# Optimization experiments

Measured on AMD Instinct MI355X. Metric: run time of the kernel, lower is better.

## Reference

```python
import jax, jax.numpy as jnp
import numpy as np
import math

E = 1024
H = 16
D = E // H  # 64
B, T, S = 4, 1024, 1024


def setup_inputs() -> dict:
    key = jax.random.key(0)
    ks = jax.random.split(key, 10)
    sd = 1.0 / math.sqrt(D)
    se = 1.0 / math.sqrt(E)
    return {
        "query": jax.random.normal(ks[0], (B, T, E), jnp.float32),
        "paragraph_encoding": jax.random.normal(ks[1], (S, E), jnp.float32),
        "Wq": jax.random.normal(ks[2], (D, D), jnp.float32) * sd,
        "bq": jax.random.normal(ks[3], (D,), jnp.float32) * sd,
        "Wk": jax.random.normal(ks[4], (D, D), jnp.float32) * sd,
        "bk": jax.random.normal(ks[5], (D,), jnp.float32) * sd,
        "Wv": jax.random.normal(ks[6], (D, D), jnp.float32) * sd,
        "bv": jax.random.normal(ks[7], (D,), jnp.float32) * sd,
        "Wout": jax.random.normal(ks[8], (E, E), jnp.float32) * se,
        "bout": jax.random.normal(ks[9], (E,), jnp.float32) * se,
    }


def reference(query, paragraph_encoding, Wq, bq, Wk, bk, Wv, bv, Wout, bout):
    b, t, _ = query.shape
    s = paragraph_encoding.shape[0]
    # [B, H, T, D]
    q = query.reshape(b, t, H, D).transpose(0, 2, 1, 3)
    # [H, S, D] -- key/value shared across batch
    p = paragraph_encoding.reshape(s, H, D).transpose(1, 0, 2)
    # per-head linear projections (torch Linear: x @ W.T + b)
    q = q @ Wq.T + bq
    k = p @ Wk.T + bk
    v = p @ Wv.T + bv
    # scores scaled by sqrt(embed_size), NOT head_dim (faithful to source)
    scores = jnp.einsum("bhtd,hsd->bhts", q, k) / math.sqrt(E)
    attn = jax.nn.softmax(scores, axis=-1)
    # (mask is None in this configuration; masking would occur AFTER softmax)
    context = jnp.einsum("bhts,hsd->bhtd", attn, v)
    context = context.transpose(0, 2, 1, 3).reshape(b, t, E)
    return context @ Wout.T + bout
```

## Files before the change

kernel.cpp:

```cpp
#include <hip/hip_runtime.h>


typedef __attribute__((ext_vector_type(8))) short short8v;
typedef __attribute__((ext_vector_type(4))) short short4v;
typedef __attribute__((ext_vector_type(4))) float float4v;

#define MFMA_BF16(A, B, C) __builtin_amdgcn_mfma_f32_16x16x32_bf16(A, B, C, 0, 0, 0)

#if __has_builtin(__builtin_amdgcn_exp2f)
#define EXP2F(x) __builtin_amdgcn_exp2f(x)
#else
#define EXP2F(x) exp2f(x)
#endif

#define QSCALE 0.045084220027780106f

__device__ __forceinline__ short f2bf(float f) {
  union { float f; unsigned u; } v; v.f = f;
  unsigned r = v.u + 0x7FFFu + ((v.u >> 16) & 1u);
  return (short)(r >> 16);
}

__device__ __forceinline__ unsigned cvt_pk_bf16(float lo, float hi) {
  unsigned r;
  asm("v_cvt_pk_bf16_f32 %0, %1, %2" : "=v"(r) : "v"(lo), "v"(hi));
  return r;
}

__global__ __launch_bounds__(256) void proj_qkv(
    const float* __restrict__ query, const float* __restrict__ para,
    const float* __restrict__ Wq, const float* __restrict__ bq,
    const float* __restrict__ Wk, const float* __restrict__ bk,
    const float* __restrict__ Wv, const float* __restrict__ bv,
    const float* __restrict__ Wout,
    short* __restrict__ qs, short* __restrict__ kb, short* __restrict__ vt,
    short* __restrict__ wb) {
  const int task = blockIdx.x * 4 + (threadIdx.x >> 6);
  const int lane = threadIdx.x & 63;
  const int g = lane >> 4, c = lane & 15;

  if (task >= 6144) {
    const int j = task - 6144;
    const float* src = Wout + j * 2048;
    short* dst = wb + j * 2048;
#pragma unroll
    for (int it = 0; it < 4; ++it) {
      const int off = it * 512 + lane * 8;
      float4v x0 = *(const float4v*)(src + off);
      float4v x1 = *(const float4v*)(src + off + 4);
      short8v v = (short8v){ f2bf(x0.x), f2bf(x0.y), f2bf(x0.z), f2bf(x0.w),
                             f2bf(x1.x), f2bf(x1.y), f2bf(x1.z), f2bf(x1.w) };
      *(short8v*)(dst + off) = v;
    }
    return;
  }

  const float* W;
  const float* bias;
  const float* xrow;
  int type, h, tile, bh = 0;
  if (task < 4096) {
    type = 0; bh = task >> 6; tile = task & 63; h = bh & 15;
    xrow = query + ((bh >> 4) * 1024 + tile * 16 + c) * 1024 + h * 64;
    W = Wq; bias = bq;
  } else if (task < 5120) {
    int idx = task - 4096;
    type = 1; h = idx >> 6; tile = idx & 63;
    xrow = para + (tile * 16 + c) * 1024 + h * 64;
    W = Wk; bias = bk;
  } else {
    int idx = task - 5120;
    type = 2; h = idx >> 6; tile = idx & 63;
    xrow = para + (tile * 16 + c) * 1024 + h * 64;
    W = Wv; bias = bv;
  }

  short8v af[2];
#pragma unroll
  for (int kh = 0; kh < 2; ++kh) {
    const float* xp = xrow + kh * 32 + g * 8;
    float4v x0 = *(const float4v*)xp;
    float4v x1 = *(const float4v*)(xp + 4);
    af[kh] = (short8v){ f2bf(x0.x), f2bf(x0.y), f2bf(x0.z), f2bf(x0.w),
                        f2bf(x1.x), f2bf(x1.y), f2bf(x1.z), f2bf(x1.w) };
  }

#pragma unroll
  for (int dn = 0; dn < 4; ++dn) {
    float4v acc = (float4v){0.f, 0.f, 0.f, 0.f};
#pragma unroll
    for (int kh = 0; kh < 2; ++kh) {
      const float* wp = W + (dn * 16 + c) * 64 + kh * 32 + g * 8;
      float4v w0 = *(const float4v*)wp;
      float4v w1 = *(const float4v*)(wp + 4);
      short8v bfr = (short8v){ f2bf(w0.x), f2bf(w0.y), f2bf(w0.z), f2bf(w0.w),
                               f2bf(w1.x), f2bf(w1.y), f2bf(w1.z), f2bf(w1.w) };
      acc = MFMA_BF16(af[kh], bfr, acc);
    }
    const float bc = bias[dn * 16 + c];
    if (type == 0) {
#pragma unroll
      for (int r = 0; r < 4; ++r) {
        const int t = tile * 16 + 4 * g + r;
        qs[(bh * 1024 + t) * 64 + dn * 16 + c] = f2bf((acc[r] + bc) * QSCALE);
      }
    } else if (type == 1) {
#pragma unroll
      for (int r = 0; r < 4; ++r) {
        const int s = tile * 16 + 4 * g + r;
        kb[(h * 1024 + s) * 64 + dn * 16 + c] = f2bf(acc[r] + bc);
      }
    } else {
      short4v pk = (short4v){ f2bf(acc[0] + bc), f2bf(acc[1] + bc),
                              f2bf(acc[2] + bc), f2bf(acc[3] + bc) };
      *(short4v*)(vt + (h * 64 + dn * 16 + c) * 1024 + tile * 16 + 4 * g) = pk;
    }
  }
}

__global__ __launch_bounds__(256, 4) void attn_fwd(
    const short* __restrict__ qs, const short* __restrict__ kb,
    const short* __restrict__ vt, short* __restrict__ ctx) {
  __shared__ __align__(16) short kv[2][4096];
  __shared__ __align__(16) short plds[4][2][16][40];
  const int tid = threadIdx.x;
  const int w = tid >> 6;
  const int lane = tid & 63;
  const int g = lane >> 4, c = lane & 15;
  const int bh = blockIdx.x & 63;
  const int b = bh >> 4, h = bh & 15;
  const int t0 = (blockIdx.x >> 6) * 128 + w * 32;

  const int kr = tid >> 3, kq = (tid & 7) ^ (kr & 7);
  const char* ksrc = (const char*)(kb + h * 65536) + kr * 128 + kq * 16;
  const int vd = tid >> 2, vq = (tid & 3) ^ ((vd >> 1) & 3);
  const char* vsrc = (const char*)(vt + h * 65536) + vd * 2048 + vq * 16;
  char* kdst = (char*)&kv[0][0] + tid * 16;
  char* vdst = (char*)&kv[0][0] + 4096 + tid * 16;

  int koff[2][2];
#pragma unroll
  for (int sm = 0; sm < 2; ++sm)
#pragma unroll
    for (int kh = 0; kh < 2; ++kh)
      koff[sm][kh] = (sm * 16 + c) * 128 + (((kh * 4 + g) ^ (c & 7)) * 16);
  int voff[4];
#pragma unroll
  for (int nt = 0; nt < 4; ++nt)
    voff[nt] = 4096 + (nt * 16 + c) * 64 + ((g ^ ((c >> 1) & 3)) * 16);

  const short* qbase = qs + (bh * 1024 + t0) * 64;
  short8v qf[2][2];
#pragma unroll
  for (int tn = 0; tn < 2; ++tn)
#pragma unroll
    for (int kh = 0; kh < 2; ++kh)
      qf[tn][kh] = *(const short8v*)(qbase + (tn * 16 + c) * 64 + kh * 32 + g * 8);

  float4v cacc[2][4];
#pragma unroll
  for (int tn = 0; tn < 2; ++tn)
#pragma unroll
    for (int nt = 0; nt < 4; ++nt)
      cacc[tn][nt] = (float4v){0.f, 0.f, 0.f, 0.f};
  float4v dacc[2];
  dacc[0] = (float4v){0.f, 0.f, 0.f, 0.f};
  dacc[1] = (float4v){0.f, 0.f, 0.f, 0.f};
  const short obf = (short)0x3F80;
  const short8v ones = (short8v){obf, obf, obf, obf, obf, obf, obf, obf};

  short8v sk = *(const short8v*)ksrc;
  short8v sv = *(const short8v*)vsrc;
  *(short8v*)kdst = sk;
  *(short8v*)vdst = sv;

  const char* kv0 = (const char*)&kv[0][0];
  for (int i = 0; i < 32; ++i) {
    __syncthreads();
    if (i < 31) {
      sk = *(const short8v*)(ksrc + (i + 1) * 4096);
      sv = *(const short8v*)(vsrc + (i + 1) * 64);
    }

    const char* kvb = kv0 + (i & 1) * 8192;
    short8v kf[2][2];
#pragma unroll
    for (int sm = 0; sm < 2; ++sm)
#pragma unroll
      for (int kh = 0; kh < 2; ++kh)
        kf[sm][kh] = *(const short8v*)(kvb + koff[sm][kh]);
    short8v vf[4];
#pragma unroll
    for (int nt = 0; nt < 4; ++nt)
      vf[nt] = *(const short8v*)(kvb + voff[nt]);

#pragma unroll
    for (int sm = 0; sm < 2; ++sm)
#pragma unroll
      for (int tn = 0; tn < 2; ++tn) {
        float4v z = (float4v){0.f, 0.f, 0.f, 0.f};
        z = MFMA_BF16(kf[sm][0], qf[tn][0], z);
        z = MFMA_BF16(kf[sm][1], qf[tn][1], z);
        const float p0 = EXP2F(z[0]);
        const float p1 = EXP2F(z[1]);
        const float p2 = EXP2F(z[2]);
        const float p3 = EXP2F(z[3]);
        uint2 u;
        u.x = cvt_pk_bf16(p0, p1);
        u.y = cvt_pk_bf16(p2, p3);
        *(uint2*)&plds[w][tn][c][sm * 16 + 4 * g] = u;
      }

    asm volatile("" ::: "memory");

    short8v pa[2];
#pragma unroll
    for (int tn = 0; tn < 2; ++tn)
      pa[tn] = *(const short8v*)&plds[w][tn][c][g * 8];

#pragma unroll
    for (int tn = 0; tn < 2; ++tn) {
#pragma unroll
      for (int nt = 0; nt < 4; ++nt)
        cacc[tn][nt] = MFMA_BF16(pa[tn], vf[nt], cacc[tn][nt]);
      dacc[tn] = MFMA_BF16(pa[tn], ones, dacc[tn]);
    }

    asm volatile("" ::: "memory");

    if (i < 31) {
      *(short8v*)(kdst + ((i + 1) & 1) * 8192) = sk;
      *(short8v*)(vdst + ((i + 1) & 1) * 8192) = sv;
    }
  }

  const int orow0 = b * 1024 + t0;
#pragma unroll
  for (int tn = 0; tn < 2; ++tn) {
    float inv[4];
#pragma unroll
    for (int r = 0; r < 4; ++r) inv[r] = 1.0f / dacc[tn][r];
#pragma unroll
    for (int nt = 0; nt < 4; ++nt)
#pragma unroll
      for (int r = 0; r < 4; ++r) {
        const int row = orow0 + tn * 16 + 4 * g + r;
        ctx[row * 1024 + h * 64 + nt * 16 + c] = f2bf(cacc[tn][nt][r] * inv[r]);
      }
  }
}

__global__ __launch_bounds__(256, 2) void out_proj(
    const short* __restrict__ ctx, const short* __restrict__ wb,
    const float* __restrict__ bout, float* __restrict__ out) {
  __shared__ __align__(16) short ab[2][6144];
  const int tid = threadIdx.x;
  const int w = tid >> 6;
  const int lane = tid & 63;
  const int g = lane >> 4, c = lane & 15;
  const int wm = w >> 1, wn = w & 1;
  const int mblk = (blockIdx.x & 31) * 128;
  const int n0 = (blockIdx.x >> 5) * 64;

  const int srow = tid >> 2;
  const int sq = (tid & 3) ^ ((srow >> 1) & 3);
  const char* asrc0 = (const char*)ctx + (mblk + srow) * 2048 + sq * 16;
  const char* asrc1 = asrc0 + 64 * 2048;
  const char* bsrc  = (const char*)wb + (n0 + srow) * 2048 + sq * 16;
  char* adst0 = (char*)&ab[0][0] + tid * 16;
  char* adst1 = (char*)&ab[0][0] + 4096 + tid * 16;
  char* bdst  = (char*)&ab[0][0] + 8192 + tid * 16;

  const int sw = (g ^ ((c >> 1) & 3)) * 16;
  int aoff[4], boff[2];
#pragma unroll
  for (int mt = 0; mt < 4; ++mt)
    aoff[mt] = (wm * 64 + mt * 16 + c) * 64 + sw;
#pragma unroll
  for (int nt = 0; nt < 2; ++nt)
    boff[nt] = 8192 + (wn * 32 + nt * 16 + c) * 64 + sw;

  float4v acc[4][2];
#pragma unroll
  for (int mt = 0; mt < 4; ++mt)
#pragma unroll
    for (int nt = 0; nt < 2; ++nt)
      acc[mt][nt] = (float4v){0.f, 0.f, 0.f, 0.f};

  short8v sa0 = *(const short8v*)asrc0;
  short8v sa1 = *(const short8v*)asrc1;
  short8v sbv = *(const short8v*)bsrc;
  *(short8v*)adst0 = sa0;
  *(short8v*)adst1 = sa1;
  *(short8v*)bdst = sbv;

  const char* ab0 = (const char*)&ab[0][0];
  for (int i = 0; i < 32; ++i) {
    __syncthreads();
    if (i < 31) {
      sa0 = *(const short8v*)(asrc0 + (i + 1) * 64);
      sa1 = *(const short8v*)(asrc1 + (i + 1) * 64);
      sbv = *(const short8v*)(bsrc + (i + 1) * 64);
    }
    const char* abb = ab0 + (i & 1) * 12288;
    short8v a[4], bb[2];
#pragma unroll
    for (int mt = 0; mt < 4; ++mt)
      a[mt] = *(const short8v*)(abb + aoff[mt]);
#pragma unroll
    for (int nt = 0; nt < 2; ++nt)
      bb[nt] = *(const short8v*)(abb + boff[nt]);
#pragma unroll
    for (int mt = 0; mt < 4; ++mt)
#pragma unroll
      for (int nt = 0; nt < 2; ++nt)
        acc[mt][nt] = MFMA_BF16(a[mt], bb[nt], acc[mt][nt]);
    if (i < 31) {
      *(short8v*)(adst0 + ((i + 1) & 1) * 12288) = sa0;
      *(short8v*)(adst1 + ((i + 1) & 1) * 12288) = sa1;
      *(short8v*)(bdst + ((i + 1) & 1) * 12288) = sbv;
    }
  }

  float bs[2];
#pragma unroll
  for (int nt = 0; nt < 2; ++nt) bs[nt] = bout[n0 + wn * 32 + nt * 16 + c];

  const int m0 = mblk + wm * 64;
#pragma unroll
  for (int mt = 0; mt < 4; ++mt)
#pragma unroll
    for (int nt = 0; nt < 2; ++nt)
#pragma unroll
      for (int r = 0; r < 4; ++r)
        out[(m0 + mt * 16 + 4 * g + r) * 1024 + n0 + wn * 32 + nt * 16 + c] =
            acc[mt][nt][r] + bs[nt];
}

extern "C" void kernel_launch(void* const* d_in, const int* in_sizes, int n_in,
                              void* d_out, int out_size, void* d_ws, size_t ws_size,
                              hipStream_t stream) {
  const float* query = (const float*)d_in[0];
  const float* para  = (const float*)d_in[1];
  const float* Wq = (const float*)d_in[2];
  const float* bq = (const float*)d_in[3];
  const float* Wk = (const float*)d_in[4];
  const float* bk = (const float*)d_in[5];
  const float* Wv = (const float*)d_in[6];
  const float* bv = (const float*)d_in[7];
  const float* Wout = (const float*)d_in[8];
  const float* bout = (const float*)d_in[9];
  float* out = (float*)d_out;

  char* ws = (char*)d_ws;
  short* qs  = (short*)(ws);
  short* kb  = (short*)(ws + (8u  << 20));
  short* vt  = (short*)(ws + (10u << 20));
  short* ctx = (short*)(ws + (12u << 20));
  short* wb  = (short*)(ws + (20u << 20));

  proj_qkv<<<dim3(1664), dim3(256), 0, stream>>>(query, para, Wq, bq, Wk, bk,
                                                 Wv, bv, Wout, qs, kb, vt, wb);
  attn_fwd<<<dim3(512), dim3(256), 0, stream>>>(qs, kb, vt, ctx);
  out_proj<<<dim3(512), dim3(256), 0, stream>>>(ctx, wb, bout, out);
}
```

Measured before the change: 65.15 us.

## Fuse Q projection into attention kernel, drop Q workspace round trip

Moves the per-head Q projection out of the projection kernel and into the attention kernel prologue. Each wave loads its fp32 query rows, projects them with MFMA, and stages the scaled bf16 result in the K/V shared-memory buffer before loading fragments. This removes the global write and re-read of the bf16 Q tensor and shrinks the projection grid. In exchange, the attention kernel does extra prologue work, adds a barrier, and rereads Wq per block.

```diff
diff --git a/kernel.cpp b/kernel.cpp
--- a/kernel.cpp
+++ b/kernel.cpp
@@ -28,19 +28,17 @@
 }
 
 __global__ __launch_bounds__(256) void proj_qkv(
-    const float* __restrict__ query, const float* __restrict__ para,
-    const float* __restrict__ Wq, const float* __restrict__ bq,
+    const float* __restrict__ para,
     const float* __restrict__ Wk, const float* __restrict__ bk,
     const float* __restrict__ Wv, const float* __restrict__ bv,
     const float* __restrict__ Wout,
-    short* __restrict__ qs, short* __restrict__ kb, short* __restrict__ vt,
-    short* __restrict__ wb) {
+    short* __restrict__ kb, short* __restrict__ vt, short* __restrict__ wb) {
   const int task = blockIdx.x * 4 + (threadIdx.x >> 6);
   const int lane = threadIdx.x & 63;
   const int g = lane >> 4, c = lane & 15;
 
-  if (task >= 6144) {
-    const int j = task - 6144;
+  if (task >= 2048) {
+    const int j = task - 2048;
     const float* src = Wout + j * 2048;
     short* dst = wb + j * 2048;
 #pragma unroll
@@ -55,25 +53,12 @@
     return;
   }
 
-  const float* W;
-  const float* bias;
-  const float* xrow;
-  int type, h, tile, bh = 0;
-  if (task < 4096) {
-    type = 0; bh = task >> 6; tile = task & 63; h = bh & 15;
-    xrow = query + ((bh >> 4) * 1024 + tile * 16 + c) * 1024 + h * 64;
-    W = Wq; bias = bq;
-  } else if (task < 5120) {
-    int idx = task - 4096;
-    type = 1; h = idx >> 6; tile = idx & 63;
-    xrow = para + (tile * 16 + c) * 1024 + h * 64;
-    W = Wk; bias = bk;
-  } else {
-    int idx = task - 5120;
-    type = 2; h = idx >> 6; tile = idx & 63;
-    xrow = para + (tile * 16 + c) * 1024 + h * 64;
-    W = Wv; bias = bv;
-  }
+  const int type = (task < 1024) ? 1 : 2;
+  const int idx = (task < 1024) ? task : task - 1024;
+  const int h = idx >> 6, tile = idx & 63;
+  const float* xrow = para + (tile * 16 + c) * 1024 + h * 64;
+  const float* W = (type == 1) ? Wk : Wv;
+  const float* bias = (type == 1) ? bk : bv;
 
   short8v af[2];
 #pragma unroll
@@ -98,13 +83,7 @@
       acc = MFMA_BF16(af[kh], bfr, acc);
     }
     const float bc = bias[dn * 16 + c];
-    if (type == 0) {
-#pragma unroll
-      for (int r = 0; r < 4; ++r) {
-        const int t = tile * 16 + 4 * g + r;
-        qs[(bh * 1024 + t) * 64 + dn * 16 + c] = f2bf((acc[r] + bc) * QSCALE);
-      }
-    } else if (type == 1) {
+    if (type == 1) {
 #pragma unroll
       for (int r = 0; r < 4; ++r) {
         const int s = tile * 16 + 4 * g + r;
@@ -119,8 +98,10 @@
 }
 
 __global__ __launch_bounds__(256, 4) void attn_fwd(
-    const short* __restrict__ qs, const short* __restrict__ kb,
-    const short* __restrict__ vt, short* __restrict__ ctx) {
+    const float* __restrict__ query,
+    const float* __restrict__ Wq, const float* __restrict__ bq,
+    const short* __restrict__ kb, const short* __restrict__ vt,
+    short* __restrict__ ctx) {
   __shared__ __align__(16) short kv[2][4096];
   __shared__ __align__(16) short plds[4][2][16][40];
   const int tid = threadIdx.x;
@@ -131,6 +112,50 @@
   const int b = bh >> 4, h = bh & 15;
   const int t0 = (blockIdx.x >> 6) * 128 + w * 32;
 
+  short* qreg = (short*)&kv[0][0] + w * 2048;
+#pragma unroll
+  for (int tn = 0; tn < 2; ++tn) {
+    const float* xrow = query + (b * 1024 + t0 + tn * 16 + c) * 1024 + h * 64;
+    short8v af[2];
+#pragma unroll
+    for (int kh = 0; kh < 2; ++kh) {
+      const float* xp = xrow + kh * 32 + g * 8;
+      float4v x0 = *(const float4v*)xp;
+      float4v x1 = *(const float4v*)(xp + 4);
+      af[kh] = (short8v){ f2bf(x0.x), f2bf(x0.y), f2bf(x0.z), f2bf(x0.w),
+                          f2bf(x1.x), f2bf(x1.y), f2bf(x1.z), f2bf(x1.w) };
+    }
+#pragma unroll
+    for (int dn = 0; dn < 4; ++dn) {
+      float4v acc = (float4v){0.f, 0.f, 0.f, 0.f};
+#pragma unroll
+      for (int kh = 0; kh < 2; ++kh) {
+        const float* wp = Wq + (dn * 16 + c) * 64 + kh * 32 + g * 8;
+        float4v w0 = *(const float4v*)wp;
+        float4v w1 = *(const float4v*)(wp + 4);
+        short8v bfr = (short8v){ f2bf(w0.x), f2bf(w0.y), f2bf(w0.z), f2bf(w0.w),
+                                 f2bf(w1.x), f2bf(w1.y), f2bf(w1.z), f2bf(w1.w) };
+        acc = MFMA_BF16(af[kh], bfr, acc);
+      }
+      const float bc = bq[dn * 16 + c];
+#pragma unroll
+      for (int r = 0; r < 4; ++r)
+        qreg[(tn * 16 + 4 * g + r) * 64 + dn * 16 + c] =
+            f2bf((acc[r] + bc) * QSCALE);
+    }
+  }
+
+  asm volatile("" ::: "memory");
+
+  short8v qf[2][2];
+#pragma unroll
+  for (int tn = 0; tn < 2; ++tn)
+#pragma unroll
+    for (int kh = 0; kh < 2; ++kh)
+      qf[tn][kh] = *(const short8v*)(qreg + (tn * 16 + c) * 64 + kh * 32 + g * 8);
+
+  __syncthreads();
+
   const int kr = tid >> 3, kq = (tid & 7) ^ (kr & 7);
   const char* ksrc = (const char*)(kb + h * 65536) + kr * 128 + kq * 16;
   const int vd = tid >> 2, vq = (tid & 3) ^ ((vd >> 1) & 3);
@@ -148,14 +173,6 @@
 #pragma unroll
   for (int nt = 0; nt < 4; ++nt)
     voff[nt] = 4096 + (nt * 16 + c) * 64 + ((g ^ ((c >> 1) & 3)) * 16);
-
-  const short* qbase = qs + (bh * 1024 + t0) * 64;
-  short8v qf[2][2];
-#pragma unroll
-  for (int tn = 0; tn < 2; ++tn)
-#pragma unroll
-    for (int kh = 0; kh < 2; ++kh)
-      qf[tn][kh] = *(const short8v*)(qbase + (tn * 16 + c) * 64 + kh * 32 + g * 8);
 
   float4v cacc[2][4];
 #pragma unroll
@@ -353,14 +370,13 @@
   float* out = (float*)d_out;
 
   char* ws = (char*)d_ws;
-  short* qs  = (short*)(ws);
   short* kb  = (short*)(ws + (8u  << 20));
   short* vt  = (short*)(ws + (10u << 20));
   short* ctx = (short*)(ws + (12u << 20));
   short* wb  = (short*)(ws + (20u << 20));
 
-  proj_qkv<<<dim3(1664), dim3(256), 0, stream>>>(query, para, Wq, bq, Wk, bk,
-                                                 Wv, bv, Wout, qs, kb, vt, wb);
-  attn_fwd<<<dim3(512), dim3(256), 0, stream>>>(qs, kb, vt, ctx);
+  proj_qkv<<<dim3(640), dim3(256), 0, stream>>>(para, Wk, bk, Wv, bv, Wout,
+                                                kb, vt, wb);
+  attn_fwd<<<dim3(512), dim3(256), 0, stream>>>(query, Wq, bq, kb, vt, ctx);
   out_proj<<<dim3(512), dim3(256), 0, stream>>>(ctx, wb, bout, out);
 }
```

Measured after the change: 63.73 us (median of 2 runs). 2.2% less time.
